# Kernel tuning notes

Hardware: AMD Instinct MI355X
Metric: run time of the kernel (lower is better)

## Reference

```python
import jax, jax.numpy as jnp
import numpy as np

B, S, QD, DM, H = 8, 4096, 4, 1024, 16
HD = DM // H
NROT = 4
EPS_LN = 1e-5


def layer_norm(x, g, b):
    m = x.mean(axis=-1, keepdims=True)
    v = ((x - m) ** 2).mean(axis=-1, keepdims=True)
    return (x - m) / jnp.sqrt(v + EPS_LN) * g + b


def quat_normalize(q):
    return q / (jnp.linalg.norm(q, axis=-1, keepdims=True) + 1e-8)


def quat_multiply(a, b):
    w1, x1, y1, z1 = a[..., 0], a[..., 1], a[..., 2], a[..., 3]
    w2, x2, y2, z2 = b[..., 0], b[..., 1], b[..., 2], b[..., 3]
    return jnp.stack([
        w1 * w2 - x1 * x2 - y1 * y2 - z1 * z2,
        w1 * x2 + x1 * w2 + y1 * z2 - z1 * y2,
        w1 * y2 - x1 * z2 + y1 * w2 + z1 * x2,
        w1 * z2 + x1 * y2 - y1 * x2 + z1 * w2,
    ], axis=-1)


def quat_conjugate(q):
    return q * jnp.array([1.0, -1.0, -1.0, -1.0], dtype=q.dtype)


def unit_quaternion(theta):  # theta: [3]
    c0, c1, c2 = jnp.cos(theta[0] / 2), jnp.cos(theta[1] / 2), jnp.cos(theta[2] / 2)
    s0, s1, s2 = jnp.sin(theta[0] / 2), jnp.sin(theta[1] / 2), jnp.sin(theta[2] / 2)
    q = jnp.stack([c0 * c1 * c2, s0 * c1 * c2, c0 * s1 * c2, c0 * c1 * s2])
    return quat_normalize(q)


def fractal_alpha(x):  # x: [B, S, DM] -> alpha: [B]
    xf = x.reshape(x.shape[0], -1)
    ps = jnp.abs(jnp.fft.rfft(xf, axis=-1)) ** 2  # [B, N/2+1]
    freqs = jnp.fft.rfftfreq(xf.shape[-1]).astype(x.dtype)
    w = ((freqs > 0.01) & (freqs < 0.5)).astype(x.dtype)
    n = w.sum()
    log_k = jnp.log(freqs + 1e-10)
    log_P = jnp.log(ps + 1e-10)
    mk = (w * log_k).sum() / n
    mP = (w * log_P).sum(axis=-1) / n  # [B]
    dk = (log_k - mk)
    cov = (w * dk * (log_P - mP[:, None])).sum(axis=-1)
    var = (w * dk * dk).sum()
    beta = -cov / (var + 1e-10)
    D = jnp.clip((3.0 - beta) / 2.0, 0.5, 1.5)
    # alpha(D) = alpha_base*(1 + lambda*(D - D_e)/D_e), base=1.0, lambda=0.8, D_e=1.0
    return jnp.clip(1.0 * (1.0 + 0.8 * (D - 1.0)), 0.1, 3.0)


def spectral_attention(x, alpha_base, phase_shift, W_attn_out, b_attn_out, ln_g, ln_b):
    # x: [B, S, DM]
    alpha = jax.lax.stop_gradient(fractal_alpha(x))  # [B]  (torch.no_grad)
    xh = x.reshape(B, S, H, HD).transpose(0, 2, 1, 3)  # [B, H, S, HD]
    x_fft = jnp.fft.fft(xh, axis=2)  # complex [B, H, S, HD]
    freqs = jnp.fft.fftfreq(S).astype(x.dtype)  # [S]
    log_k = jnp.log(jnp.abs(freqs) + 1e-8)
    log_kn = (log_k - log_k.mean()) / (jnp.std(log_k, ddof=1) + 1e-8)
    gelu_k = jax.nn.gelu(log_kn, approximate=False)  # [S]
    # phase[b,h,s] = alpha_base[h]*alpha[b]*gelu_k[s] + phase_shift[h]
    phase = (alpha_base[None, :, None] * alpha[:, None, None] * gelu_k[None, None, :]
             + phase_shift[None, :, None])  # [B, H, S]
    kernel = jnp.exp(1j * phase.astype(jnp.float32))[..., None]  # [B, H, S, 1]
    x_filt = jnp.fft.ifft(x_fft * kernel, axis=2).real  # [B, H, S, HD]
    out = x_filt.transpose(0, 2, 1, 3).reshape(B, S, DM)
    out = out @ W_attn_out + b_attn_out  # out_proj; dropout = identity (eval)
    return layer_norm(x + out, ln_g, ln_b)


def so4_evolution(q, theta_L, theta_R):  # q: [B, S, 4]
    out = q
    for i in range(NROT):
        qL = unit_quaternion(theta_L[i])
        qR_conj = quat_conjugate(unit_quaternion(theta_R[i]))
        out = quat_multiply(quat_multiply(jnp.broadcast_to(qL, out.shape), out),
                            jnp.broadcast_to(qR_conj, out.shape))
        out = quat_normalize(out)
    return out


def setup_inputs() -> dict:
    key = jax.random.key(0)
    ks = jax.random.split(key, 24)
    def rn(k, shape, scale=0.02):
        return jax.random.normal(k, shape, dtype=jnp.float32) * scale
    return {
        "x": jax.random.normal(ks[0], (B, S, QD), dtype=jnp.float32),
        "W_in": rn(ks[1], (QD, DM)), "b_in": jnp.zeros((DM,), jnp.float32),
        "alpha_base": jnp.ones((H,), jnp.float32),
        "phase_shift": jnp.zeros((H,), jnp.float32),
        "W_attn_out": rn(ks[2], (DM, DM)), "b_attn_out": jnp.zeros((DM,), jnp.float32),
        "ln_attn_g": jnp.ones((DM,), jnp.float32), "ln_attn_b": jnp.zeros((DM,), jnp.float32),
        "W_out": rn(ks[3], (DM, QD)), "b_out": jnp.zeros((QD,), jnp.float32),
        "theta_L": rn(ks[4], (NROT, 3), 0.1), "theta_R": rn(ks[5], (NROT, 3), 0.1),
        "W_ff1": rn(ks[6], (QD, 4 * QD)), "b_ff1": jnp.zeros((4 * QD,), jnp.float32),
        "W_ff2": rn(ks[7], (4 * QD, QD)), "b_ff2": jnp.zeros((QD,), jnp.float32),
        "n1_g": jnp.ones((QD,), jnp.float32), "n1_b": jnp.zeros((QD,), jnp.float32),
        "n2_g": jnp.ones((QD,), jnp.float32), "n2_b": jnp.zeros((QD,), jnp.float32),
        "n3_g": jnp.ones((QD,), jnp.float32), "n3_b": jnp.zeros((QD,), jnp.float32),
    }


def reference(x, W_in, b_in, alpha_base, phase_shift, W_attn_out, b_attn_out,
              ln_attn_g, ln_attn_b, W_out, b_out, theta_L, theta_R,
              W_ff1, b_ff1, W_ff2, b_ff2, n1_g, n1_b, n2_g, n2_b, n3_g, n3_b):
    x_proj = x @ W_in + b_in  # [B, S, DM]
    attn = spectral_attention(x_proj, alpha_base, phase_shift, W_attn_out, b_attn_out,
                              ln_attn_g, ln_attn_b)
    attn_quat = attn @ W_out + b_out  # [B, S, 4]
    h = quat_normalize(layer_norm(x + attn_quat, n1_g, n1_b))
    evolved = so4_evolution(h, theta_L, theta_R)
    h = quat_normalize(layer_norm(h + evolved, n2_g, n2_b))
    ff = jax.nn.gelu(h @ W_ff1 + b_ff1, approximate=False) @ W_ff2 + b_ff2
    h = quat_normalize(layer_norm(h + ff, n3_g, n3_b))
    return h
```

## Files before the change

kernel.cpp:

```cpp
#include <hip/hip_runtime.h>
#include <hip/hip_bf16.h>
#include <math.h>


#define DEV static __device__ __forceinline__
typedef unsigned int uint32;
typedef unsigned short u16;

typedef __attribute__((ext_vector_type(8))) _Float16 f16x8;
typedef __attribute__((ext_vector_type(4))) float f32x4;
typedef __attribute__((ext_vector_type(2))) unsigned int u32x2;

DEV float2 cmulf(float2 a, float2 b) {
  return make_float2(a.x * b.x - a.y * b.y, a.x * b.y + a.y * b.x);
}
DEV u16 f2h(float f) {
  union { _Float16 h; u16 u; } v;
  v.h = (_Float16)f;
  return v.u;
}
DEV float h2f(uint32 u) {
  union { u16 s; _Float16 h; } v;
  v.s = (u16)u;
  return (float)v.h;
}
DEV void glds16(void* lds, const void* g) {
  __builtin_amdgcn_global_load_lds((const __attribute__((address_space(1))) unsigned int*)g,
                                   (__attribute__((address_space(3))) unsigned int*)lds, 16, 0, 0);
}
DEV void wave_sync() {
  asm volatile("s_waitcnt lgkmcnt(0)" ::: "memory");
  __builtin_amdgcn_sched_barrier(0);
}
DEV int dr10(int v) {
  int r = (int)(__brev((unsigned)v) >> 22);
  return ((r & 0x155) << 1) | ((r & 0x2AA) >> 1);
}
DEV int dr12(int v) {
  int r = (int)(__brev((unsigned)v) >> 20);
  return ((r & 0x555) << 1) | ((r & 0xAAA) >> 1);
}

constexpr float CR_C[16] = {
  1.0f, 0.980785280403230f, 0.923879532511287f, 0.831469612302545f,
  0.707106781186548f, 0.555570233019602f, 0.382683432365090f, 0.195090322016128f,
  0.0f, -0.195090322016128f, -0.382683432365090f, -0.555570233019602f,
  -0.707106781186548f, -0.831469612302545f, -0.923879532511287f, -0.980785280403230f };
constexpr float CR_S[16] = {
  0.0f, 0.195090322016128f, 0.382683432365090f, 0.555570233019602f,
  0.707106781186548f, 0.831469612302545f, 0.923879532511287f, 0.980785280403230f,
  1.0f, 0.980785280403230f, 0.923879532511287f, 0.831469612302545f,
  0.707106781186548f, 0.555570233019602f, 0.382683432365090f, 0.195090322016128f };

template<int L, int NLOG, int NSUB, bool WL>
DEV void dif4_stages(float2* F, int lg) {
  #pragma unroll
  for (int st = 0; st < NLOG / 2; ++st) {
    const int qlog = NLOG - 2 - 2 * st;
    const int q = 1 << qlog;
    float bs, bc;
    __sincosf((float)(lg & (q - 1)) * (-1.57079632679489661923f / (float)q), &bs, &bc);
    const float2 base = make_float2(bc, bs);
    #pragma unroll
    for (int u = 0; u < NSUB * (1 << (NLOG - 2)) / L; ++u) {
      const int sub = (u * L) >> (NLOG - 2);
      const int bf = ((u * L) & ((1 << (NLOG - 2)) - 1)) + lg;
      const int jj = ((u * L) % q) * 8 / q;
      const int i1 = (sub << NLOG) + ((bf >> qlog) << (qlog + 2)) + (bf & (q - 1));
      float2 x0 = F[i1], x1 = F[i1 + q], x2 = F[i1 + 2 * q], x3 = F[i1 + 3 * q];
      float2 s0 = make_float2(x0.x + x2.x, x0.y + x2.y);
      float2 s1 = make_float2(x0.x - x2.x, x0.y - x2.y);
      float2 s2 = make_float2(x1.x + x3.x, x1.y + x3.y);
      float2 dq = make_float2(x1.x - x3.x, x1.y - x3.y);
      float2 s3 = make_float2(dq.y, -dq.x);
      F[i1] = make_float2(s0.x + s2.x, s0.y + s2.y);
      if (qlog == 0) {
        F[i1 + 1] = make_float2(s1.x + s3.x, s1.y + s3.y);
        F[i1 + 2] = make_float2(s0.x - s2.x, s0.y - s2.y);
        F[i1 + 3] = make_float2(s1.x - s3.x, s1.y - s3.y);
      } else {
        const float2 tf1 = (jj == 0) ? base : cmulf(base, make_float2(CR_C[jj], -CR_S[jj]));
        const float2 tf2 = cmulf(tf1, tf1);
        const float2 tf3 = cmulf(tf2, tf1);
        F[i1 + q]     = cmulf(make_float2(s1.x + s3.x, s1.y + s3.y), tf1);
        F[i1 + 2 * q] = cmulf(make_float2(s0.x - s2.x, s0.y - s2.y), tf2);
        F[i1 + 3 * q] = cmulf(make_float2(s1.x - s3.x, s1.y - s3.y), tf3);
      }
    }
    if (WL) wave_sync(); else __syncthreads();
  }
}

template<int L, int NLOG, int NSUB, bool WL>
DEV void dit4_stages(float2* F, int lg) {
  #pragma unroll
  for (int st = 0; st < NLOG / 2; ++st) {
    const int qlog = 2 * st;
    const int q = 1 << qlog;
    float bs, bc;
    __sincosf((float)(lg & (q - 1)) * (1.57079632679489661923f / (float)q), &bs, &bc);
    const float2 base = make_float2(bc, bs);
    #pragma unroll
    for (int u = 0; u < NSUB * (1 << (NLOG - 2)) / L; ++u) {
      const int sub = (u * L) >> (NLOG - 2);
      const int bf = ((u * L) & ((1 << (NLOG - 2)) - 1)) + lg;
      const int jj = ((u * L) % q) * 8 / q;
      const int i1 = (sub << NLOG) + ((bf >> qlog) << (qlog + 2)) + (bf & (q - 1));
      float2 b0 = F[i1];
      float2 b1 = F[i1 + q], b2 = F[i1 + 2 * q], b3 = F[i1 + 3 * q];
      if (qlog != 0) {
        const float2 tf1 = (jj == 0) ? base : cmulf(base, make_float2(CR_C[jj], CR_S[jj]));
        const float2 tf2 = cmulf(tf1, tf1);
        const float2 tf3 = cmulf(tf2, tf1);
        b1 = cmulf(b1, tf1);
        b2 = cmulf(b2, tf2);
        b3 = cmulf(b3, tf3);
      }
      float2 t0 = make_float2(b0.x + b2.x, b0.y + b2.y);
      float2 t1 = make_float2(b0.x - b2.x, b0.y - b2.y);
      float2 t2 = make_float2(b1.x + b3.x, b1.y + b3.y);
      float2 dq = make_float2(b1.x - b3.x, b1.y - b3.y);
      float2 t3 = make_float2(-dq.y, dq.x);
      F[i1]         = make_float2(t0.x + t2.x, t0.y + t2.y);
      F[i1 + q]     = make_float2(t1.x + t3.x, t1.y + t3.y);
      F[i1 + 2 * q] = make_float2(t0.x - t2.x, t0.y - t2.y);
      F[i1 + 3 * q] = make_float2(t1.x - t3.x, t1.y - t3.y);
    }
    if (WL) wave_sync(); else __syncthreads();
  }
}

DEV float4 qmul4(float4 a, float4 b) {
  return make_float4(
    a.x * b.x - a.y * b.y - a.z * b.z - a.w * b.w,
    a.x * b.y + a.y * b.x + a.z * b.w - a.w * b.z,
    a.x * b.z - a.y * b.w + a.z * b.x + a.w * b.y,
    a.x * b.w + a.y * b.z - a.z * b.y + a.w * b.x);
}
DEV float4 qne(float4 q) {
  float n = sqrtf(q.x * q.x + q.y * q.y + q.z * q.z + q.w * q.w) + 1e-8f;
  float r = 1.0f / n;
  return make_float4(q.x * r, q.y * r, q.z * r, q.w * r);
}

__global__ __launch_bounds__(512) void kx_fr_pass1(const float* __restrict__ x,
    const float* __restrict__ W_in, const float* __restrict__ b_in,
    float2* __restrict__ zmid) {
  __shared__ float2 fb[8 * 1028];
  const int t = threadIdx.x, l = t & 63, w = t >> 6;
  const int btile = blockIdx.x, bz = blockIdx.y;
  const int bcol = btile * 8 + w;
  const int d = 2 * (bcol & 511);
  const int soff = bcol >> 9;
  const float w00 = W_in[d],     w10 = W_in[1024 + d], w20 = W_in[2048 + d], w30 = W_in[3072 + d];
  const float w01 = W_in[d + 1], w11 = W_in[1025 + d], w21 = W_in[2049 + d], w31 = W_in[3073 + d];
  const float bi0 = b_in[d], bi1 = b_in[d + 1];
  const float* xb = x + (size_t)bz * 4096 * 4;
  float2* fbw = fb + w * 1028;
  #pragma unroll
  for (int i = 0; i < 16; ++i) {
    int a = i * 64 + l;
    int s = 4 * a + soff;
    float4 xv = *(const float4*)(xb + (size_t)s * 4);
    float z0 = fmaf(xv.x, w00, fmaf(xv.y, w10, fmaf(xv.z, w20, fmaf(xv.w, w30, bi0))));
    float z1 = fmaf(xv.x, w01, fmaf(xv.y, w11, fmaf(xv.z, w21, fmaf(xv.w, w31, bi1))));
    fbw[a] = make_float2(z0, z1);
  }
  wave_sync();
  dif4_stages<64, 10, 1, true>(fbw, l);
  __syncthreads();
  float2* dst = zmid + (size_t)bz * (1024 * 2048);
  #pragma unroll
  for (int i = 0; i < 16; ++i) {
    int idx = i * 512 + t;
    int w8 = idx & 7, cnat = idx >> 3;
    float2 v = fb[w8 * 1028 + dr10(cnat)];
    dst[(size_t)cnat * 2048 + btile * 8 + w8] = v;
  }
}

DEV float block_reduce128(float* red, int t, float v) {
  red[t] = v; __syncthreads();
  for (int s = 64; s; s >>= 1) { if (t < s) red[t] += red[t + s]; __syncthreads(); }
  float r = red[0]; __syncthreads();
  return r;
}

__global__ __launch_bounds__(128) void kx_fr_pass2(const float2* __restrict__ zmid,
    float* __restrict__ partials, float* __restrict__ sparts) {
  __shared__ float2 fb[2 * 2052];
  __shared__ float red[128];
  const int t = threadIdx.x, l = t & 63, w = t >> 6;
  const int cg = blockIdx.x, bz = blockIdx.y;
  const int c = (cg == 0) ? (w ? 512 : 0) : (w ? (1024 - cg) : cg);
  const float2* src = zmid + ((size_t)bz * 1024 + c) * 2048;
  float2* fbc = fb + w * 2052;
  float2 rot[4], stp4;
  {
    float sn, cs;
    __sincosf((float)(l * c) * (-6.28318530717958647692f / 2097152.0f), &sn, &cs);
    rot[0] = make_float2(cs, sn);
    float2 stp;
    __sincosf((float)c * (-6.28318530717958647692f / 32768.0f), &sn, &cs);
    stp = make_float2(cs, sn);
    rot[1] = cmulf(rot[0], stp);
    float2 stp2 = cmulf(stp, stp);
    rot[2] = cmulf(rot[0], stp2);
    rot[3] = cmulf(rot[1], stp2);
    stp4 = cmulf(stp2, stp2);
  }
  float2 zr[32];
  #pragma unroll
  for (int i = 0; i < 32; ++i) {
    int bb = i * 64 + l;
    zr[i] = cmulf(src[bb], rot[i & 3]);
    rot[i & 3] = cmulf(rot[i & 3], stp4);
  }
  {
    float bs, bc;
    __sincosf((float)l * (-3.14159265358979323846f / 1024.0f), &bs, &bc);
    const float2 b2 = make_float2(bc, bs);
    #pragma unroll
    for (int u = 0; u < 16; ++u) {
      const float2 tf = (u == 0) ? b2 : cmulf(b2, make_float2(CR_C[u], -CR_S[u]));
      int i1 = u * 64 + l;
      float2 a0 = zr[u], a1 = zr[u + 16];
      fbc[i1] = make_float2(a0.x + a1.x, a0.y + a1.y);
      fbc[i1 + 1024] = cmulf(make_float2(a0.x - a1.x, a0.y - a1.y), tf);
    }
    wave_sync();
  }
  dif4_stages<64, 10, 2, true>(fbc, l);
  __syncthreads();
  float t0 = 0.f, t1 = 0.f, s0 = 0.f, s1 = 0.f, s2 = 0.f;
  if (cg != 0) {
    const float2* fbm = fb + (1 - w) * 2052;
    float2 pw[32];
    pw[0] = make_float2(1.f, 0.f);
    {
      float sn, cs;
      __sincosf(-3.14159265358979323846f / 2048.0f, &sn, &cs);
      float2 w1 = make_float2(cs, sn);
      #pragma unroll
      for (int j = 1; j < 32; ++j) pw[j] = cmulf(pw[j - 1], w1);
    }
    const int drl = (l & 3) * 256 + ((l >> 2) & 3) * 64 + ((l >> 4) & 3) * 16;
    float2 base2;
    {
      float sn, cs;
      __sincosf((float)drl * (-3.14159265358979323846f / 1024.0f), &sn, &cs);
      float2 lf = make_float2(cs, sn);
      __sincosf((float)c * (-6.28318530717958647692f / 4194304.0f), &sn, &cs);
      base2 = cmulf(make_float2(cs, sn), lf);
    }
    #pragma unroll
    for (int i = 0; i < 32; ++i) {
      const int p = i * 64 + l;
      const int dri = (i & 3) * 4 + ((i >> 2) & 3);
      const int top = i >> 4;
      const int dd = 2 * (drl + dri) + top;
      float2 Zk = fbc[p];
      float2 Zm = fbm[2047 - p];
      float2 E = make_float2(0.5f * (Zk.x + Zm.x), 0.5f * (Zk.y - Zm.y));
      float2 A = make_float2(Zk.x - Zm.x, Zk.y + Zm.y);
      float2 O = make_float2(0.5f * A.y, -0.5f * A.x);
      float2 urot = cmulf(base2, pw[2 * dri + top]);
      float2 U = cmulf(urot, O);
      float Xr = E.x + U.x, Xi = E.y + U.y;
      float P = Xr * Xr + Xi * Xi;
      int k = c + (dd << 10);
      float fr = (float)k * (1.0f / 4194304.0f);
      if (fr > 0.01f && fr < 0.5f) {
        float lp = __logf(P + 1e-10f);
        float lk = __logf(fr + 1e-10f);
        t0 += lp; t1 += lk * lp;
        s0 += 1.0f; s1 += lk; s2 += lk * lk;
      }
    }
  } else {
    const float2* fbm = fbc;
    float2 urot;
    {
      float sn, cs;
      __sincosf((float)(c + l * 1024) * (-6.28318530717958647692f / 4194304.0f), &sn, &cs);
      urot = make_float2(cs, sn);
    }
    const float2 ustp = make_float2(0.995184726672197f, -0.0980171403295606f);
    #pragma unroll
    for (int i = 0; i < 32; ++i) {
      int dd = i * 64 + l;
      int md = (c == 0) ? ((2048 - dd) & 2047) : (2047 - dd);
      int pk = ((dd & 1) << 10) | dr10(dd >> 1);
      int pm = ((md & 1) << 10) | dr10(md >> 1);
      float2 Zk = fbc[pk];
      float2 Zm = fbm[pm];
      float2 E = make_float2(0.5f * (Zk.x + Zm.x), 0.5f * (Zk.y - Zm.y));
      float2 A = make_float2(Zk.x - Zm.x, Zk.y + Zm.y);
      float2 O = make_float2(0.5f * A.y, -0.5f * A.x);
      float2 U = cmulf(urot, O);
      float Xr = E.x + U.x, Xi = E.y + U.y;
      float P = Xr * Xr + Xi * Xi;
      int k = c + (dd << 10);
      float fr = (float)k * (1.0f / 4194304.0f);
      if (fr > 0.01f && fr < 0.5f) {
        float lp = __logf(P + 1e-10f);
        float lk = __logf(fr + 1e-10f);
        t0 += lp; t1 += lk * lp;
        s0 += 1.0f; s1 += lk; s2 += lk * lk;
      }
      urot = cmulf(urot, ustp);
    }
  }
  float T0 = block_reduce128(red, t, t0);
  float T1 = block_reduce128(red, t, t1);
  if (t == 0) {
    partials[((size_t)bz * 512 + cg) * 2 + 0] = T0;
    partials[((size_t)bz * 512 + cg) * 2 + 1] = T1;
  }
  if (bz == 0) {
    float S0 = block_reduce128(red, t, s0);
    float S1 = block_reduce128(red, t, s1);
    float S2 = block_reduce128(red, t, s2);
    if (t == 0) { sparts[cg * 3] = S0; sparts[cg * 3 + 1] = S1; sparts[cg * 3 + 2] = S2; }
  }
}

DEV float block_reduce512(float* sh, int t, float v) {
  sh[t] = v; __syncthreads();
  for (int s = 256; s; s >>= 1) { if (t < s) sh[t] += sh[t + s]; __syncthreads(); }
  float r = sh[0]; __syncthreads();
  return r;
}

__global__ __launch_bounds__(512) void kx_finalize(const float* __restrict__ partials,
    const float* __restrict__ sparts, float* __restrict__ alpha, float* __restrict__ gelu) {
  __shared__ float sh[512];
  __shared__ float lk[4096];
  const int t = threadIdx.x;
  float S0 = block_reduce512(sh, t, sparts[t * 3 + 0]);
  float S1 = block_reduce512(sh, t, sparts[t * 3 + 1]);
  float S2 = block_reduce512(sh, t, sparts[t * 3 + 2]);
  float mk = S1 / S0;
  float var = S2 - mk * S1;
  for (int b = 0; b < 8; ++b) {
    float T0 = block_reduce512(sh, t, partials[((size_t)b * 512 + t) * 2 + 0]);
    float T1 = block_reduce512(sh, t, partials[((size_t)b * 512 + t) * 2 + 1]);
    if (t == 0) {
      float cov = T1 - mk * T0;
      float beta = -cov / (var + 1e-10f);
      float D = fminf(fmaxf((3.0f - beta) * 0.5f, 0.5f), 1.5f);
      alpha[b] = fminf(fmaxf(1.0f + 0.8f * (D - 1.0f), 0.1f), 3.0f);
    }
  }
  for (int s = t; s < 4096; s += 512) {
    int m = (s < 2048) ? s : (4096 - s);
    lk[s] = logf((float)m * (1.0f / 4096.0f) + 1e-8f);
  }
  __syncthreads();
  float ls = 0.f;
  for (int s = t; s < 4096; s += 512) ls += lk[s];
  float mean = block_reduce512(sh, t, ls) * (1.0f / 4096.0f);
  float vs = 0.f;
  for (int s = t; s < 4096; s += 512) { float dv = lk[s] - mean; vs += dv * dv; }
  float sd = sqrtf(block_reduce512(sh, t, vs) * (1.0f / 4095.0f));
  for (int k = t; k < 2049; k += 512) {
    float xn = (lk[k] - mean) / (sd + 1e-8f);
    gelu[k] = 0.5f * xn * (1.0f + erff(xn * 0.70710678118654752440f));
  }
}

__global__ __launch_bounds__(256) void kx_gains(const float* __restrict__ alpha,
    const float* __restrict__ gelu, const float* __restrict__ abase,
    const float* __restrict__ pshift, const float* __restrict__ thL,
    const float* __restrict__ thR, float* __restrict__ gains, float* __restrict__ qlr) {
  const int bh = blockIdx.x;
  const float aa = abase[bh & 15] * alpha[bh >> 4];
  const float ps = pshift[bh & 15];
  for (int k = threadIdx.x; k < 2049; k += 256)
    gains[(size_t)bh * 2064 + k] = cosf(fmaf(aa, gelu[k], ps));
  if (bh == 0 && threadIdx.x == 0) {
    float4 QL = make_float4(1.f, 0.f, 0.f, 0.f);
    float4 QRC = make_float4(1.f, 0.f, 0.f, 0.f);
    for (int it = 0; it < 4; ++it) {
      float s0, c0, s1, c1, s2, c2;
      sincosf(0.5f * thL[it * 3 + 0], &s0, &c0);
      sincosf(0.5f * thL[it * 3 + 1], &s1, &c1);
      sincosf(0.5f * thL[it * 3 + 2], &s2, &c2);
      float4 qL = qne(make_float4(c0 * c1 * c2, s0 * c1 * c2, c0 * s1 * c2, c0 * c1 * s2));
      QL = qmul4(qL, QL);
      sincosf(0.5f * thR[it * 3 + 0], &s0, &c0);
      sincosf(0.5f * thR[it * 3 + 1], &s1, &c1);
      sincosf(0.5f * thR[it * 3 + 2], &s2, &c2);
      float4 qR = qne(make_float4(c0 * c1 * c2, s0 * c1 * c2, c0 * s1 * c2, c0 * c1 * s2));
      QRC = qmul4(QRC, make_float4(qR.x, -qR.y, -qR.z, -qR.w));
    }
    *(float4*)qlr = QL;
    *(float4*)(qlr + 4) = QRC;
  }
}

__global__ __launch_bounds__(256) void kx_wt(const float* __restrict__ W, u16* __restrict__ Wt) {
  __shared__ float tile[64][65];
  const int t = threadIdx.x;
  const int nt = blockIdx.x, dt = blockIdx.y;
  #pragma unroll
  for (int i = 0; i < 16; ++i) {
    int idx = i * 256 + t;
    int r = idx >> 6, cc = idx & 63;
    tile[r][cc] = W[(size_t)(dt * 64 + r) * 1024 + nt * 64 + cc];
  }
  __syncthreads();
  #pragma unroll
  for (int i = 0; i < 2; ++i) {
    int task = i * 256 + t;
    int nl = task >> 3, g = task & 7;
    union { u16 h[8]; uint4 v; } pk;
    #pragma unroll
    for (int k = 0; k < 8; ++k) pk.h[k] = f2h(tile[g * 8 + k][nl]);
    size_t idx = (size_t)(nt * 64 + nl) * 1024 + dt * 64 + ((g ^ (nl & 7)) << 3);
    *(uint4*)(Wt + idx) = pk.v;
  }
}

__global__ __launch_bounds__(256) void kx_filter(const float* __restrict__ x,
    const float* __restrict__ W_in, const float* __restrict__ b_in,
    const float* __restrict__ gains, u16* __restrict__ xfh) {
  __shared__ float2 fb[2 * 4096];
  const int t = threadIdx.x;
  const int lg = t & 127, q = t >> 7;
  const int g = blockIdx.x, h = blockIdx.y, bz = blockIdx.z;
  const int d0 = h * 64 + g * 4 + q * 2;
  const float* gn = gains + ((size_t)bz * 16 + h) * 2064;
  const float wa0 = W_in[d0],     wa1 = W_in[1024 + d0], wa2 = W_in[2048 + d0], wa3 = W_in[3072 + d0];
  const float wb0 = W_in[d0 + 1], wb1 = W_in[1025 + d0], wb2 = W_in[2049 + d0], wb3 = W_in[3073 + d0];
  const float bia = b_in[d0], bib = b_in[d0 + 1];
  const float* xb = x + (size_t)bz * 4096 * 4;
  float2* fbg = fb + q * 4096;
  #pragma unroll
  for (int i = 0; i < 32; ++i) {
    int s = i * 128 + lg;
    float4 xv = *(const float4*)(xb + (size_t)s * 4);
    float za = fmaf(xv.x, wa0, fmaf(xv.y, wa1, fmaf(xv.z, wa2, fmaf(xv.w, wa3, bia))));
    float zb = fmaf(xv.x, wb0, fmaf(xv.y, wb1, fmaf(xv.z, wb2, fmaf(xv.w, wb3, bib))));
    fbg[s] = make_float2(za, zb);
  }
  __syncthreads();
  dif4_stages<128, 12, 1, false>(fbg, lg);
  #pragma unroll
  for (int i = 0; i < 32; ++i) {
    int p = i * 128 + lg;
    int k = dr12(p);
    int km = (k < 2048) ? k : (4096 - k);
    float gk = gn[km];
    float2 v = fbg[p];
    fbg[p] = make_float2(v.x * gk, v.y * gk);
  }
  __syncthreads();
  dit4_stages<128, 12, 1, false>(fbg, lg);
  u16* rowa = xfh + ((size_t)bz * 1024 + d0) * 4096;
  u16* rowb = rowa + 4096;
  const float sc = 1.0f / 4096.0f;
  #pragma unroll
  for (int i = 0; i < 32; ++i) {
    int s = i * 128 + lg;
    float2 v = fbg[s];
    rowa[s] = f2h(v.x * sc);
    rowb[s] = f2h(v.y * sc);
  }
}

__global__ __launch_bounds__(256) void kx_a16(const u16* __restrict__ XFh, u16* __restrict__ Aswz) {
  __shared__ uint32 tl[64][129];
  const int t = threadIdx.x;
  const int dt = blockIdx.x, st = blockIdx.y, bh = blockIdx.z;
  const u16* src = XFh + ((size_t)bh * 1024 + dt * 64) * 4096 + st * 256;
  #pragma unroll
  for (int i = 0; i < 8; ++i) {
    int dl = i * 8 + (t >> 5);
    int sl = (t & 31) * 8;
    uint4 v = *(const uint4*)(src + (size_t)dl * 4096 + sl);
    tl[dl][(t & 31) * 4 + 0] = v.x;
    tl[dl][(t & 31) * 4 + 1] = v.y;
    tl[dl][(t & 31) * 4 + 2] = v.z;
    tl[dl][(t & 31) * 4 + 3] = v.w;
  }
  __syncthreads();
  u16* dstb = Aswz + ((size_t)bh * 4096 + st * 256) * 1024 + dt * 64;
  #pragma unroll
  for (int j = 0; j < 8; ++j) {
    int task = j * 256 + t;
    int sl = task >> 3, g = task & 7;
    int sp = sl >> 1, sh = (sl & 1) * 16;
    uint4 ov;
    uint32 w0, w1;
    w0 = tl[g * 8 + 0][sp]; w1 = tl[g * 8 + 1][sp];
    ov.x = ((w0 >> sh) & 0xFFFFu) | (((w1 >> sh) & 0xFFFFu) << 16);
    w0 = tl[g * 8 + 2][sp]; w1 = tl[g * 8 + 3][sp];
    ov.y = ((w0 >> sh) & 0xFFFFu) | (((w1 >> sh) & 0xFFFFu) << 16);
    w0 = tl[g * 8 + 4][sp]; w1 = tl[g * 8 + 5][sp];
    ov.z = ((w0 >> sh) & 0xFFFFu) | (((w1 >> sh) & 0xFFFFu) << 16);
    w0 = tl[g * 8 + 6][sp]; w1 = tl[g * 8 + 7][sp];
    ov.w = ((w0 >> sh) & 0xFFFFu) | (((w1 >> sh) & 0xFFFFu) << 16);
    *(uint4*)(dstb + (size_t)sl * 1024 + ((g ^ (sl & 7)) << 3)) = ov;
  }
}

__global__ __launch_bounds__(256) void kx_gemm(const u16* __restrict__ A,
    const u16* __restrict__ Bw, u16* __restrict__ C) {
  __shared__ u16 sm[32768];
  const int t = threadIdx.x, l = t & 63, w = t >> 6;
  const int wm = w >> 1, wn = w & 1;
  const int id = blockIdx.x;
  const int wg = (id & 7) * 256 + (id >> 3);
  const int bm = wg >> 3, bn = wg & 7;
  const int bh = bm >> 5;
  const u16* Ab = A + ((size_t)(bh * 4096 + (bm & 31) * 128)) * 1024;
  const u16* Bb = Bw + (size_t)(bn * 128) * 1024;
  const int fr = l & 15;
  const int lr = l >> 3, lg = l & 7;
  f32x4 acc[4][4];
  #pragma unroll
  for (int m = 0; m < 4; ++m)
    #pragma unroll
    for (int n = 0; n < 4; ++n) acc[m][n] = (f32x4){0.f, 0.f, 0.f, 0.f};

  #define STAGE(KT, BUF) { \
    u16* Ad = sm + (BUF) * 8192; \
    u16* Bd = sm + 16384 + (BUF) * 8192; \
    _Pragma("unroll") \
    for (int j = 0; j < 4; ++j) { \
      int qq = j * 4 + w; \
      glds16((void*)(Ad + qq * 512), Ab + (size_t)(qq * 8 + lr) * 1024 + (KT) * 64 + lg * 8); \
      glds16((void*)(Bd + qq * 512), Bb + (size_t)(qq * 8 + lr) * 1024 + (KT) * 64 + lg * 8); \
    } }

  STAGE(0, 0);
  __syncthreads();
  for (int kt = 0; kt < 16; ++kt) {
    const int cur = kt & 1;
    if (kt < 15) STAGE(kt + 1, cur ^ 1);
    const u16* Ac = sm + cur * 8192;
    const u16* Bc = sm + 16384 + cur * 8192;
    #pragma unroll
    for (int kk = 0; kk < 2; ++kk) {
      const int g8r = kk * 4 + (l >> 4);
      f16x8 af[4], bf[4];
      #pragma unroll
      for (int m = 0; m < 4; ++m) {
        int s = wm * 64 + m * 16 + fr;
        af[m] = *(const f16x8*)&Ac[s * 64 + ((g8r ^ (s & 7)) << 3)];
      }
      #pragma unroll
      for (int n = 0; n < 4; ++n) {
        int nn = wn * 64 + n * 16 + fr;
        bf[n] = *(const f16x8*)&Bc[nn * 64 + ((g8r ^ (nn & 7)) << 3)];
      }
      #pragma unroll
      for (int m = 0; m < 4; ++m)
        #pragma unroll
        for (int n = 0; n < 4; ++n)
          acc[m][n] = __builtin_amdgcn_mfma_f32_16x16x32_f16(af[m], bf[n], acc[m][n], 0, 0, 0);
    }
    __syncthreads();
  }
  float* Cs = (float*)sm;
  const int rl4 = (l >> 4) * 4;
  #pragma unroll
  for (int m = 0; m < 4; ++m) {
    int rbase = wm * 64 + m * 16 + rl4;
    #pragma unroll
    for (int n = 0; n < 4; ++n) {
      int cc = wn * 64 + n * 16 + fr;
      #pragma unroll
      for (int e = 0; e < 4; ++e) {
        int r = rbase + e;
        Cs[r * 128 + (cc ^ (((r >> 2) & 3) << 3))] = acc[m][n][e];
      }
    }
  }
  __syncthreads();
  u16* cgp = C + (size_t)(bm * 128) * 1024 + bn * 128;
  #pragma unroll
  for (int it = 0; it < 16; ++it) {
    int idx = it * 256 + t;
    int r = idx >> 5, c4 = (idx & 31) * 4;
    f32x4 v = *(const f32x4*)&Cs[r * 128 + (c4 ^ (((r >> 2) & 3) << 3))];
    u32x2 pv;
    pv.x = (uint32)f2h(v.x) | ((uint32)f2h(v.y) << 16);
    pv.y = (uint32)f2h(v.z) | ((uint32)f2h(v.w) << 16);
    __builtin_nontemporal_store(pv, (u32x2*)(cgp + (size_t)r * 1024 + c4));
  }
}

DEV float wred64(float v) {
  #pragma unroll
  for (int m = 32; m; m >>= 1) v += __shfl_xor(v, m);
  return v;
}
DEV float4 ln4q(float4 v, const float* g, const float* b) {
  float m = 0.25f * (v.x + v.y + v.z + v.w);
  float a0 = v.x - m, a1 = v.y - m, a2 = v.z - m, a3 = v.w - m;
  float var = 0.25f * (a0 * a0 + a1 * a1 + a2 * a2 + a3 * a3);
  float rs = 1.0f / sqrtf(var + 1e-5f);
  return make_float4(a0 * rs * g[0] + b[0], a1 * rs * g[1] + b[1],
                     a2 * rs * g[2] + b[2], a3 * rs * g[3] + b[3]);
}
DEV float gelu1(float v) { return 0.5f * v * (1.0f + erff(v * 0.70710678118654752440f)); }

__global__ __launch_bounds__(256) void kx_tail(const u16* __restrict__ G,
    const float* __restrict__ x, const float* __restrict__ W_in, const float* __restrict__ b_in,
    const float* __restrict__ b_attn, const float* __restrict__ lng, const float* __restrict__ lnb,
    const float* __restrict__ W_out, const float* __restrict__ b_out,
    const float* __restrict__ qlr,
    const float* __restrict__ Wf1, const float* __restrict__ bff1,
    const float* __restrict__ Wf2, const float* __restrict__ bff2,
    const float* __restrict__ n1g, const float* __restrict__ n1b,
    const float* __restrict__ n2g, const float* __restrict__ n2b,
    const float* __restrict__ n3g, const float* __restrict__ n3b,
    float* __restrict__ out) {
  const int l = threadIdx.x & 63, w = threadIdx.x >> 6;
  const size_t rg = (size_t)blockIdx.x * 4 + w;
  const float4 x4 = *(const float4*)(x + rg * 4);
  float4 tv[4];
  float lsum = 0.f;
  #pragma unroll
  for (int j = 0; j < 4; ++j) {
    int dd = j * 256 + l * 4;
    uint2 gv = *(const uint2*)(G + rg * 1024 + dd);
    float4 g4 = make_float4(h2f(gv.x & 0xFFFFu), h2f(gv.x >> 16),
                            h2f(gv.y & 0xFFFFu), h2f(gv.y >> 16));
    float4 w0 = *(const float4*)(W_in + dd);
    float4 w1 = *(const float4*)(W_in + 1024 + dd);
    float4 w2 = *(const float4*)(W_in + 2048 + dd);
    float4 w3 = *(const float4*)(W_in + 3072 + dd);
    float4 bi = *(const float4*)(b_in + dd);
    float4 ba = *(const float4*)(b_attn + dd);
    float4 o;
    o.x = g4.x + bi.x + ba.x + x4.x * w0.x + x4.y * w1.x + x4.z * w2.x + x4.w * w3.x;
    o.y = g4.y + bi.y + ba.y + x4.x * w0.y + x4.y * w1.y + x4.z * w2.y + x4.w * w3.y;
    o.z = g4.z + bi.z + ba.z + x4.x * w0.z + x4.y * w1.z + x4.z * w2.z + x4.w * w3.z;
    o.w = g4.w + bi.w + ba.w + x4.x * w0.w + x4.y * w1.w + x4.z * w2.w + x4.w * w3.w;
    tv[j] = o;
    lsum += o.x + o.y + o.z + o.w;
  }
  const float mean = wred64(lsum) * (1.0f / 1024.0f);
  float vsum = 0.f;
  #pragma unroll
  for (int j = 0; j < 4; ++j) {
    float a0 = tv[j].x - mean, a1 = tv[j].y - mean, a2 = tv[j].z - mean, a3 = tv[j].w - mean;
    vsum += a0 * a0 + a1 * a1 + a2 * a2 + a3 * a3;
  }
  const float rstd = 1.0f / sqrtf(wred64(vsum) * (1.0f / 1024.0f) + 1e-5f);
  float4 aq = make_float4(0.f, 0.f, 0.f, 0.f);
  #pragma unroll
  for (int j = 0; j < 4; ++j) {
    int dd = j * 256 + l * 4;
    float4 gg = *(const float4*)(lng + dd);
    float4 bb = *(const float4*)(lnb + dd);
    float av[4];
    av[0] = (tv[j].x - mean) * rstd * gg.x + bb.x;
    av[1] = (tv[j].y - mean) * rstd * gg.y + bb.y;
    av[2] = (tv[j].z - mean) * rstd * gg.z + bb.z;
    av[3] = (tv[j].w - mean) * rstd * gg.w + bb.w;
    #pragma unroll
    for (int e = 0; e < 4; ++e) {
      float4 wr = *(const float4*)(W_out + (size_t)(dd + e) * 4);
      aq.x = fmaf(av[e], wr.x, aq.x);
      aq.y = fmaf(av[e], wr.y, aq.y);
      aq.z = fmaf(av[e], wr.z, aq.z);
      aq.w = fmaf(av[e], wr.w, aq.w);
    }
  }
  aq.x = wred64(aq.x) + b_out[0];
  aq.y = wred64(aq.y) + b_out[1];
  aq.z = wred64(aq.z) + b_out[2];
  aq.w = wred64(aq.w) + b_out[3];
  float4 q1 = make_float4(x4.x + aq.x, x4.y + aq.y, x4.z + aq.z, x4.w + aq.w);
  float4 hq = qne(ln4q(q1, n1g, n1b));
  const float4 QL = *(const float4*)qlr;
  const float4 QRC = *(const float4*)(qlr + 4);
  float4 o = qne(qmul4(qmul4(QL, hq), QRC));
  float4 h2 = qne(ln4q(make_float4(hq.x + o.x, hq.y + o.y, hq.z + o.z, hq.w + o.w), n2g, n2b));
  float ffx = 0.f, ffy = 0.f, ffz = 0.f, ffw = 0.f;
  if (l < 16) {
    float uv = bff1[l] + h2.x * Wf1[l] + h2.y * Wf1[16 + l] + h2.z * Wf1[32 + l] + h2.w * Wf1[48 + l];
    uv = gelu1(uv);
    float4 w2r = *(const float4*)(Wf2 + l * 4);
    ffx = uv * w2r.x; ffy = uv * w2r.y; ffz = uv * w2r.z; ffw = uv * w2r.w;
  }
  ffx = wred64(ffx) + bff2[0];
  ffy = wred64(ffy) + bff2[1];
  ffz = wred64(ffz) + bff2[2];
  ffw = wred64(ffw) + bff2[3];
  float4 h3 = qne(ln4q(make_float4(h2.x + ffx, h2.y + ffy, h2.z + ffz, h2.w + ffw), n3g, n3b));
  if (l == 0) *(float4*)(out + rg * 4) = h3;
}

extern "C" void kernel_launch(void* const* d_in, const int* in_sizes, int n_in,
                              void* d_out, int out_size, void* d_ws, size_t ws_size,
                              hipStream_t stream) {
  (void)in_sizes; (void)n_in; (void)out_size;
  const float* x      = (const float*)d_in[0];
  const float* W_in   = (const float*)d_in[1];
  const float* b_in   = (const float*)d_in[2];
  const float* abase  = (const float*)d_in[3];
  const float* pshift = (const float*)d_in[4];
  const float* Wattn  = (const float*)d_in[5];
  const float* battn  = (const float*)d_in[6];
  const float* lng    = (const float*)d_in[7];
  const float* lnb    = (const float*)d_in[8];
  const float* Wout   = (const float*)d_in[9];
  const float* bout   = (const float*)d_in[10];
  const float* thL    = (const float*)d_in[11];
  const float* thR    = (const float*)d_in[12];
  const float* Wf1    = (const float*)d_in[13];
  const float* bff1   = (const float*)d_in[14];
  const float* Wf2    = (const float*)d_in[15];
  const float* bff2   = (const float*)d_in[16];
  const float* n1g    = (const float*)d_in[17];
  const float* n1b    = (const float*)d_in[18];
  const float* n2g    = (const float*)d_in[19];
  const float* n2b    = (const float*)d_in[20];
  const float* n3g    = (const float*)d_in[21];
  const float* n3b    = (const float*)d_in[22];

  if (ws_size < (size_t)138459204) return;
  char* ws = (char*)d_ws;
  float2* Zmid  = (float2*)ws;
  u16*   XFh    = (u16*)ws;
  u16*   Aswz   = (u16*)(ws + 67108864);
  u16*   C16    = (u16*)ws;
  u16*   W2h    = (u16*)(ws + 134217728);
  float* gainsw = (float*)(ws + 136314880);
  float* qlrw   = (float*)(ws + 137400320);
  float* partials = (float*)(ws + 138412032);
  float* sparts   = (float*)(ws + 138444800);
  float* alphaw   = (float*)(ws + 138450944);
  float* geluw    = (float*)(ws + 138451008);

  kx_fr_pass1<<<dim3(256, 8), 512, 0, stream>>>(x, W_in, b_in, Zmid);
  kx_fr_pass2<<<dim3(512, 8), 128, 0, stream>>>(Zmid, partials, sparts);
  kx_finalize<<<1, 512, 0, stream>>>(partials, sparts, alphaw, geluw);
  kx_gains<<<128, 256, 0, stream>>>(alphaw, geluw, abase, pshift, thL, thR, gainsw, qlrw);
  kx_wt<<<dim3(16, 16), 256, 0, stream>>>(Wattn, W2h);
  kx_filter<<<dim3(16, 16, 8), 256, 0, stream>>>(x, W_in, b_in, gainsw, XFh);
  kx_a16<<<dim3(16, 16, 8), 256, 0, stream>>>(XFh, Aswz);
  kx_gemm<<<2048, 256, 0, stream>>>(Aswz, W2h, C16);
  kx_tail<<<8192, 256, 0, stream>>>(C16, x, W_in, b_in, battn, lng, lnb, Wout, bout,
                                    qlrw, Wf1, bff1, Wf2, bff2,
                                    n1g, n1b, n2g, n2b, n3g, n3b, (float*)d_out);
}
```

Measured before the change: 473.6 us.

## Rewrite filter FFT as register-resident 64x64 four-step with fp16 LDS transposes

The 4096-point forward/inverse FFT in kx_filter moves from an LDS radix-4 kernel with block-wide barriers to a four-step 64x64 decomposition. Each lane holds 64 complex values in registers, applies twiddles, and transposes through LDS once per direction, with only wave-level syncs. Blocks shrink to 128 threads (one wave per channel pair) and the LDS exchange is packed as fp16 pairs. This cuts LDS traffic and barriers, but raises register pressure (64 float2 per thread) and adds fp16 rounding to the intermediate FFT data, which may hurt accuracy.

```diff
diff --git a/kernel.cpp b/kernel.cpp
--- a/kernel.cpp
+++ b/kernel.cpp
@@ -24,6 +24,9 @@
   v.s = (u16)u;
   return (float)v.h;
 }
+DEV uint32 pack2h(float a, float b) {
+  return (uint32)f2h(a) | ((uint32)f2h(b) << 16);
+}
 DEV void glds16(void* lds, const void* g) {
   __builtin_amdgcn_global_load_lds((const __attribute__((address_space(1))) unsigned int*)g,
                                    (__attribute__((address_space(3))) unsigned int*)lds, 16, 0, 0);
@@ -36,9 +39,24 @@
   int r = (int)(__brev((unsigned)v) >> 22);
   return ((r & 0x155) << 1) | ((r & 0x2AA) >> 1);
 }
-DEV int dr12(int v) {
-  int r = (int)(__brev((unsigned)v) >> 20);
-  return ((r & 0x555) << 1) | ((r & 0xAAA) >> 1);
+constexpr int dr6c(int v) {
+  return ((v & 3) << 4) | (v & 12) | ((v >> 4) & 3);
+}
+
+constexpr float CQ[17] = {
+  1.0f, 0.995184726672197f, 0.980785280403230f, 0.956940335732209f,
+  0.923879532511287f, 0.881921264348355f, 0.831469612302545f, 0.773010453362737f,
+  0.707106781186548f, 0.634393284163645f, 0.555570233019602f, 0.471396736825998f,
+  0.382683432365090f, 0.290284677254462f, 0.195090322016128f, 0.098017140329561f, 0.0f };
+constexpr float twc64(int j) {
+  return (j & 63) <= 16 ? CQ[j & 63]
+       : (j & 63) <= 32 ? -CQ[32 - (j & 63)]
+       : (j & 63) <= 48 ? -CQ[(j & 63) - 32] : CQ[64 - (j & 63)];
+}
+constexpr float tws64(int j) {
+  return (j & 63) <= 16 ? CQ[16 - (j & 63)]
+       : (j & 63) <= 32 ? CQ[(j & 63) - 16]
+       : (j & 63) <= 48 ? -CQ[48 - (j & 63)] : -CQ[(j & 63) - 48];
 }
 
 constexpr float CR_C[16] = {
@@ -51,6 +69,116 @@
   0.707106781186548f, 0.831469612302545f, 0.923879532511287f, 0.980785280403230f,
   1.0f, 0.980785280403230f, 0.923879532511287f, 0.831469612302545f,
   0.707106781186548f, 0.555570233019602f, 0.382683432365090f, 0.195090322016128f };
+
+template<int SGN>
+DEV void rdif64(float2* z) {
+  #pragma unroll
+  for (int j = 0; j < 16; ++j) {
+    float2 x0 = z[j], x1 = z[j + 16], x2 = z[j + 32], x3 = z[j + 48];
+    float2 s0 = make_float2(x0.x + x2.x, x0.y + x2.y);
+    float2 s1 = make_float2(x0.x - x2.x, x0.y - x2.y);
+    float2 s2 = make_float2(x1.x + x3.x, x1.y + x3.y);
+    float2 d  = make_float2(x1.x - x3.x, x1.y - x3.y);
+    float2 s3 = (SGN < 0) ? make_float2(d.y, -d.x) : make_float2(-d.y, d.x);
+    z[j] = make_float2(s0.x + s2.x, s0.y + s2.y);
+    const float2 tf1 = make_float2(twc64(j),     (float)SGN * tws64(j));
+    const float2 tf2 = make_float2(twc64(2 * j), (float)SGN * tws64(2 * j));
+    const float2 tf3 = make_float2(twc64(3 * j), (float)SGN * tws64(3 * j));
+    z[j + 16] = cmulf(make_float2(s1.x + s3.x, s1.y + s3.y), tf1);
+    z[j + 32] = cmulf(make_float2(s0.x - s2.x, s0.y - s2.y), tf2);
+    z[j + 48] = cmulf(make_float2(s1.x - s3.x, s1.y - s3.y), tf3);
+  }
+  #pragma unroll
+  for (int b = 0; b < 64; b += 16)
+    #pragma unroll
+    for (int j = 0; j < 4; ++j) {
+      const int i = b + j;
+      float2 x0 = z[i], x1 = z[i + 4], x2 = z[i + 8], x3 = z[i + 12];
+      float2 s0 = make_float2(x0.x + x2.x, x0.y + x2.y);
+      float2 s1 = make_float2(x0.x - x2.x, x0.y - x2.y);
+      float2 s2 = make_float2(x1.x + x3.x, x1.y + x3.y);
+      float2 d  = make_float2(x1.x - x3.x, x1.y - x3.y);
+      float2 s3 = (SGN < 0) ? make_float2(d.y, -d.x) : make_float2(-d.y, d.x);
+      z[i] = make_float2(s0.x + s2.x, s0.y + s2.y);
+      const float2 tf1 = make_float2(twc64(4 * j),  (float)SGN * tws64(4 * j));
+      const float2 tf2 = make_float2(twc64(8 * j),  (float)SGN * tws64(8 * j));
+      const float2 tf3 = make_float2(twc64(12 * j), (float)SGN * tws64(12 * j));
+      z[i + 4]  = cmulf(make_float2(s1.x + s3.x, s1.y + s3.y), tf1);
+      z[i + 8]  = cmulf(make_float2(s0.x - s2.x, s0.y - s2.y), tf2);
+      z[i + 12] = cmulf(make_float2(s1.x - s3.x, s1.y - s3.y), tf3);
+    }
+  #pragma unroll
+  for (int b = 0; b < 64; b += 4) {
+    float2 x0 = z[b], x1 = z[b + 1], x2 = z[b + 2], x3 = z[b + 3];
+    float2 s0 = make_float2(x0.x + x2.x, x0.y + x2.y);
+    float2 s1 = make_float2(x0.x - x2.x, x0.y - x2.y);
+    float2 s2 = make_float2(x1.x + x3.x, x1.y + x3.y);
+    float2 d  = make_float2(x1.x - x3.x, x1.y - x3.y);
+    float2 s3 = (SGN < 0) ? make_float2(d.y, -d.x) : make_float2(-d.y, d.x);
+    z[b]     = make_float2(s0.x + s2.x, s0.y + s2.y);
+    z[b + 1] = make_float2(s1.x + s3.x, s1.y + s3.y);
+    z[b + 2] = make_float2(s0.x - s2.x, s0.y - s2.y);
+    z[b + 3] = make_float2(s1.x - s3.x, s1.y - s3.y);
+  }
+}
+
+template<int SGN>
+DEV void rdit64(float2* z) {
+  #pragma unroll
+  for (int b = 0; b < 64; b += 4) {
+    float2 b0 = z[b], b1 = z[b + 1], b2 = z[b + 2], b3 = z[b + 3];
+    float2 t0 = make_float2(b0.x + b2.x, b0.y + b2.y);
+    float2 t1 = make_float2(b0.x - b2.x, b0.y - b2.y);
+    float2 t2 = make_float2(b1.x + b3.x, b1.y + b3.y);
+    float2 d  = make_float2(b1.x - b3.x, b1.y - b3.y);
+    float2 t3 = (SGN > 0) ? make_float2(-d.y, d.x) : make_float2(d.y, -d.x);
+    z[b]     = make_float2(t0.x + t2.x, t0.y + t2.y);
+    z[b + 1] = make_float2(t1.x + t3.x, t1.y + t3.y);
+    z[b + 2] = make_float2(t0.x - t2.x, t0.y - t2.y);
+    z[b + 3] = make_float2(t1.x - t3.x, t1.y - t3.y);
+  }
+  #pragma unroll
+  for (int b = 0; b < 64; b += 16)
+    #pragma unroll
+    for (int j = 0; j < 4; ++j) {
+      const int i = b + j;
+      const float2 tf1 = make_float2(twc64(4 * j),  (float)SGN * tws64(4 * j));
+      const float2 tf2 = make_float2(twc64(8 * j),  (float)SGN * tws64(8 * j));
+      const float2 tf3 = make_float2(twc64(12 * j), (float)SGN * tws64(12 * j));
+      float2 b0 = z[i];
+      float2 b1 = cmulf(z[i + 4], tf1);
+      float2 b2 = cmulf(z[i + 8], tf2);
+      float2 b3 = cmulf(z[i + 12], tf3);
+      float2 t0 = make_float2(b0.x + b2.x, b0.y + b2.y);
+      float2 t1 = make_float2(b0.x - b2.x, b0.y - b2.y);
+      float2 t2 = make_float2(b1.x + b3.x, b1.y + b3.y);
+      float2 d  = make_float2(b1.x - b3.x, b1.y - b3.y);
+      float2 t3 = (SGN > 0) ? make_float2(-d.y, d.x) : make_float2(d.y, -d.x);
+      z[i]      = make_float2(t0.x + t2.x, t0.y + t2.y);
+      z[i + 4]  = make_float2(t1.x + t3.x, t1.y + t3.y);
+      z[i + 8]  = make_float2(t0.x - t2.x, t0.y - t2.y);
+      z[i + 12] = make_float2(t1.x - t3.x, t1.y - t3.y);
+    }
+  #pragma unroll
+  for (int j = 0; j < 16; ++j) {
+    const float2 tf1 = make_float2(twc64(j),     (float)SGN * tws64(j));
+    const float2 tf2 = make_float2(twc64(2 * j), (float)SGN * tws64(2 * j));
+    const float2 tf3 = make_float2(twc64(3 * j), (float)SGN * tws64(3 * j));
+    float2 b0 = z[j];
+    float2 b1 = cmulf(z[j + 16], tf1);
+    float2 b2 = cmulf(z[j + 32], tf2);
+    float2 b3 = cmulf(z[j + 48], tf3);
+    float2 t0 = make_float2(b0.x + b2.x, b0.y + b2.y);
+    float2 t1 = make_float2(b0.x - b2.x, b0.y - b2.y);
+    float2 t2 = make_float2(b1.x + b3.x, b1.y + b3.y);
+    float2 d  = make_float2(b1.x - b3.x, b1.y - b3.y);
+    float2 t3 = (SGN > 0) ? make_float2(-d.y, d.x) : make_float2(d.y, -d.x);
+    z[j]      = make_float2(t0.x + t2.x, t0.y + t2.y);
+    z[j + 16] = make_float2(t1.x + t3.x, t1.y + t3.y);
+    z[j + 32] = make_float2(t0.x - t2.x, t0.y - t2.y);
+    z[j + 48] = make_float2(t1.x - t3.x, t1.y - t3.y);
+  }
+}
 
 template<int L, int NLOG, int NSUB, bool WL>
 DEV void dif4_stages(float2* F, int lg) {
@@ -91,45 +219,6 @@
   }
 }
 
-template<int L, int NLOG, int NSUB, bool WL>
-DEV void dit4_stages(float2* F, int lg) {
-  #pragma unroll
-  for (int st = 0; st < NLOG / 2; ++st) {
-    const int qlog = 2 * st;
-    const int q = 1 << qlog;
-    float bs, bc;
-    __sincosf((float)(lg & (q - 1)) * (1.57079632679489661923f / (float)q), &bs, &bc);
-    const float2 base = make_float2(bc, bs);
-    #pragma unroll
-    for (int u = 0; u < NSUB * (1 << (NLOG - 2)) / L; ++u) {
-      const int sub = (u * L) >> (NLOG - 2);
-      const int bf = ((u * L) & ((1 << (NLOG - 2)) - 1)) + lg;
-      const int jj = ((u * L) % q) * 8 / q;
-      const int i1 = (sub << NLOG) + ((bf >> qlog) << (qlog + 2)) + (bf & (q - 1));
-      float2 b0 = F[i1];
-      float2 b1 = F[i1 + q], b2 = F[i1 + 2 * q], b3 = F[i1 + 3 * q];
-      if (qlog != 0) {
-        const float2 tf1 = (jj == 0) ? base : cmulf(base, make_float2(CR_C[jj], CR_S[jj]));
-        const float2 tf2 = cmulf(tf1, tf1);
-        const float2 tf3 = cmulf(tf2, tf1);
-        b1 = cmulf(b1, tf1);
-        b2 = cmulf(b2, tf2);
-        b3 = cmulf(b3, tf3);
-      }
-      float2 t0 = make_float2(b0.x + b2.x, b0.y + b2.y);
-      float2 t1 = make_float2(b0.x - b2.x, b0.y - b2.y);
-      float2 t2 = make_float2(b1.x + b3.x, b1.y + b3.y);
-      float2 dq = make_float2(b1.x - b3.x, b1.y - b3.y);
-      float2 t3 = make_float2(-dq.y, dq.x);
-      F[i1]         = make_float2(t0.x + t2.x, t0.y + t2.y);
-      F[i1 + q]     = make_float2(t1.x + t3.x, t1.y + t3.y);
-      F[i1 + 2 * q] = make_float2(t0.x - t2.x, t0.y - t2.y);
-      F[i1 + 3 * q] = make_float2(t1.x - t3.x, t1.y - t3.y);
-    }
-    if (WL) wave_sync(); else __syncthreads();
-  }
-}
-
 DEV float4 qmul4(float4 a, float4 b) {
   return make_float4(
     a.x * b.x - a.y * b.y - a.z * b.z - a.w * b.w,
@@ -422,50 +511,103 @@
   }
 }
 
-__global__ __launch_bounds__(256) void kx_filter(const float* __restrict__ x,
+__global__ __launch_bounds__(128, 2) void kx_filter(const float* __restrict__ x,
     const float* __restrict__ W_in, const float* __restrict__ b_in,
     const float* __restrict__ gains, u16* __restrict__ xfh) {
-  __shared__ float2 fb[2 * 4096];
-  const int t = threadIdx.x;
-  const int lg = t & 127, q = t >> 7;
+  __shared__ uint32 tr[2][4096];
+  const int t = threadIdx.x, l = t & 63, wv = t >> 6;
   const int g = blockIdx.x, h = blockIdx.y, bz = blockIdx.z;
-  const int d0 = h * 64 + g * 4 + q * 2;
+  const int d0 = h * 64 + g * 4 + wv * 2;
   const float* gn = gains + ((size_t)bz * 16 + h) * 2064;
   const float wa0 = W_in[d0],     wa1 = W_in[1024 + d0], wa2 = W_in[2048 + d0], wa3 = W_in[3072 + d0];
   const float wb0 = W_in[d0 + 1], wb1 = W_in[1025 + d0], wb2 = W_in[2049 + d0], wb3 = W_in[3073 + d0];
   const float bia = b_in[d0], bib = b_in[d0 + 1];
   const float* xb = x + (size_t)bz * 4096 * 4;
-  float2* fbg = fb + q * 4096;
-  #pragma unroll
-  for (int i = 0; i < 32; ++i) {
-    int s = i * 128 + lg;
+  uint32* trw = tr[wv];
+  float2 z[64];
+  #pragma unroll
+  for (int r = 0; r < 64; ++r) {
+    int s = r * 64 + l;
     float4 xv = *(const float4*)(xb + (size_t)s * 4);
     float za = fmaf(xv.x, wa0, fmaf(xv.y, wa1, fmaf(xv.z, wa2, fmaf(xv.w, wa3, bia))));
     float zb = fmaf(xv.x, wb0, fmaf(xv.y, wb1, fmaf(xv.z, wb2, fmaf(xv.w, wb3, bib))));
-    fbg[s] = make_float2(za, zb);
-  }
-  __syncthreads();
-  dif4_stages<128, 12, 1, false>(fbg, lg);
-  #pragma unroll
-  for (int i = 0; i < 32; ++i) {
-    int p = i * 128 + lg;
-    int k = dr12(p);
-    int km = (k < 2048) ? k : (4096 - k);
-    float gk = gn[km];
-    float2 v = fbg[p];
-    fbg[p] = make_float2(v.x * gk, v.y * gk);
-  }
-  __syncthreads();
-  dit4_stages<128, 12, 1, false>(fbg, lg);
+    z[r] = make_float2(za, zb);
+  }
+  rdif64<-1>(z);
+  {
+    float sn, cs;
+    __sincosf((float)l * (-6.28318530717958647692f / 4096.0f), &sn, &cs);
+    float2 w1 = make_float2(cs, sn);
+    float2 w2 = cmulf(w1, w1);
+    float2 w4 = cmulf(w2, w2);
+    float2 tch[4] = { make_float2(1.f, 0.f), w1, w2, cmulf(w2, w1) };
+    #pragma unroll
+    for (int i = 0; i < 16; ++i) {
+      #pragma unroll
+      for (int j = 0; j < 4; ++j) {
+        const int rr = dr6c(4 * i + j);
+        z[rr] = cmulf(z[rr], tch[j]);
+      }
+      #pragma unroll
+      for (int j = 0; j < 4; ++j) tch[j] = cmulf(tch[j], w4);
+    }
+  }
+  #pragma unroll
+  for (int r = 0; r < 64; ++r) {
+    const int k1 = dr6c(r);
+    trw[k1 * 64 + ((l + k1) & 63)] = pack2h(z[r].x, z[r].y);
+  }
+  wave_sync();
+  #pragma unroll
+  for (int c = 0; c < 64; ++c) {
+    uint32 u = trw[l * 64 + ((c + l) & 63)];
+    z[c] = make_float2(h2f(u & 0xFFFFu), h2f(u >> 16));
+  }
+  wave_sync();
+  rdif64<-1>(z);
+  #pragma unroll
+  for (int r = 0; r < 64; ++r) {
+    const int k = l + (dr6c(r) << 6);
+    const int km = (k < 2048) ? k : (4096 - k);
+    const float gk = gn[km];
+    z[r] = make_float2(z[r].x * gk, z[r].y * gk);
+  }
+  rdit64<1>(z);
+  {
+    float sn, cs;
+    __sincosf((float)l * (6.28318530717958647692f / 4096.0f), &sn, &cs);
+    float2 v1 = make_float2(cs, sn);
+    float2 v2 = cmulf(v1, v1);
+    float2 v4 = cmulf(v2, v2);
+    float2 tch[4] = { make_float2(1.f, 0.f), v1, v2, cmulf(v2, v1) };
+    #pragma unroll
+    for (int i = 0; i < 16; ++i) {
+      #pragma unroll
+      for (int j = 0; j < 4; ++j)
+        z[4 * i + j] = cmulf(z[4 * i + j], tch[j]);
+      #pragma unroll
+      for (int j = 0; j < 4; ++j) tch[j] = cmulf(tch[j], v4);
+    }
+  }
+  #pragma unroll
+  for (int r = 0; r < 64; ++r)
+    trw[r * 64 + ((l + r) & 63)] = pack2h(z[r].x, z[r].y);
+  wave_sync();
+  #pragma unroll
+  for (int c = 0; c < 64; ++c) {
+    uint32 u = trw[l * 64 + ((c + l) & 63)];
+    z[c] = make_float2(h2f(u & 0xFFFFu), h2f(u >> 16));
+  }
+  wave_sync();
+  rdif64<1>(z);
   u16* rowa = xfh + ((size_t)bz * 1024 + d0) * 4096;
   u16* rowb = rowa + 4096;
   const float sc = 1.0f / 4096.0f;
   #pragma unroll
-  for (int i = 0; i < 32; ++i) {
-    int s = i * 128 + lg;
-    float2 v = fbg[s];
-    rowa[s] = f2h(v.x * sc);
-    rowb[s] = f2h(v.y * sc);
+  for (int r = 0; r < 64; ++r) {
+    const int s = (dr6c(r) << 6) + l;
+    rowa[s] = f2h(z[r].x * sc);
+    rowb[s] = f2h(z[r].y * sc);
   }
 }
 
@@ -743,7 +885,7 @@
   kx_finalize<<<1, 512, 0, stream>>>(partials, sparts, alphaw, geluw);
   kx_gains<<<128, 256, 0, stream>>>(alphaw, geluw, abase, pshift, thL, thR, gainsw, qlrw);
   kx_wt<<<dim3(16, 16), 256, 0, stream>>>(Wattn, W2h);
-  kx_filter<<<dim3(16, 16, 8), 256, 0, stream>>>(x, W_in, b_in, gainsw, XFh);
+  kx_filter<<<dim3(16, 16, 8), 128, 0, stream>>>(x, W_in, b_in, gainsw, XFh);
   kx_a16<<<dim3(16, 16, 8), 256, 0, stream>>>(XFh, Aswz);
   kx_gemm<<<2048, 256, 0, stream>>>(Aswz, W2h, C16);
   kx_tail<<<8192, 256, 0, stream>>>(C16, x, W_in, b_in, battn, lng, lnb, Wout, bout,
```

Result: no change. 468.5 us (-1.1%).
